# Optimization experiments

Measured on AMD Instinct MI355X. Metric: run time of the kernel, lower is better.

Reference implementation:

```python
import jax, jax.numpy as jnp
import numpy as np

D_MODEL = 768
N_HEAD = 12
N_BR = 4
DH = D_MODEL // N_HEAD          # 64
H_TOT = N_BR * N_HEAD           # 48
K_TOP = 4
B, T = 2, 1024


def setup_inputs() -> dict:
    key = jax.random.key(0)
    ks = jax.random.split(key, 16)
    s = 0.02
    return {
        "A": jax.random.normal(ks[0], (B, T, D_MODEL), jnp.float32),
        "X": jax.random.normal(ks[1], (B, T, D_MODEL), jnp.float32),
        "WK_w": jax.random.normal(ks[2], (D_MODEL, D_MODEL), jnp.float32) * s,
        "WK_b": jax.random.normal(ks[3], (D_MODEL,), jnp.float32) * s,
        "WQ_w": jax.random.normal(ks[4], (D_MODEL * N_BR, D_MODEL), jnp.float32) * s,
        "wedge_A": jax.random.normal(ks[5], (DH, DH), jnp.float32) * s,
        "wedge_bias": jax.random.normal(ks[6], (H_TOT, DH), jnp.float32) * s,
        "sink": jax.random.normal(ks[7], (H_TOT,), jnp.float32) * s,
        "v_nulls": jax.random.normal(ks[8], (N_BR, D_MODEL), jnp.float32) * s,
        "V1_w": jax.random.normal(ks[9], (4 * DH, DH), jnp.float32) * s,
        "V1_b": jax.random.normal(ks[10], (4 * DH,), jnp.float32) * s,
        "V2_w": jax.random.normal(ks[11], (DH, 4 * DH), jnp.float32) * s,
        "V2_b": jax.random.normal(ks[12], (DH,), jnp.float32) * s,
        "WO_w": jax.random.normal(ks[13], (N_BR, D_MODEL, D_MODEL), jnp.float32) * s,
        "WO_b": jax.random.normal(ks[14], (N_BR, D_MODEL), jnp.float32) * s,
    }


def _wedge(x, wedge_A, wedge_bias):
    # S = (A - A^T) + diag_embed(id_bias); x: [B,H,T,Dh]
    skew = wedge_A - wedge_A.T                       # [Dh,Dh]
    S = skew[None, :, :] + jax.vmap(jnp.diag)(wedge_bias)  # [H,Dh,Dh]
    return x + jnp.einsum('bhtd,hde->bhte', x, S)


def _rope(x):
    # x: [B,H,T,Dh]; halves are interleaved-split then concatenated
    t_len = x.shape[2]
    inv_freq = 1.0 / (10000.0 ** (jnp.arange(0, DH, 2, dtype=jnp.float32) / DH))
    freqs = jnp.arange(t_len, dtype=jnp.float32)[:, None] * inv_freq[None, :]  # [T,Dh/2]
    cos = jnp.cos(freqs)[None, None]
    sin = jnp.sin(freqs)[None, None]
    x1 = x[..., 0::2]
    x2 = x[..., 1::2]
    return jnp.concatenate((-x2 * sin + x1 * cos, x1 * sin + x2 * cos), axis=-1)


def reference(A, X, WK_w, WK_b, WQ_w, wedge_A, wedge_bias, sink, v_nulls,
              V1_w, V1_b, V2_w, V2_b, WO_w, WO_b):
    b, t, c = A.shape
    scale = DH ** -0.5

    q = (A @ WQ_w.T).reshape(b, t, H_TOT, DH).transpose(0, 2, 1, 3)     # [B,Htot,T,Dh]
    k_base = X @ WK_w.T + WK_b
    k = k_base.reshape(b, t, N_HEAD, DH).transpose(0, 2, 1, 3)          # [B,Nsh,T,Dh]
    k = jnp.tile(k, (1, N_BR, 1, 1))                                    # [B,Htot,T,Dh]

    q = _rope(_wedge(q, wedge_A, wedge_bias))
    k = _rope(_wedge(k, wedge_A, wedge_bias))

    scores = jnp.einsum('bhtd,bhsd->bhts', q, k) * scale                # [B,Htot,T,T]
    causal = jnp.triu(jnp.ones((t, t), dtype=bool), k=1)
    scores = jnp.where(causal[None, None], -jnp.inf, scores)

    sinks = jnp.broadcast_to(sink.reshape(1, H_TOT, 1, 1), (b, H_TOT, t, 1))
    probs_full = jax.nn.softmax(jnp.concatenate([scores, sinks], axis=-1), axis=-1)
    probs_tokens = probs_full[..., :t]
    probs_sink = probs_full[..., t:]                                    # [B,Htot,T,1]

    k_top = min(K_TOP, t)
    vals, idxs = jax.lax.top_k(probs_tokens, k_top)                     # [B,Htot,T,K]
    weights = vals / (jnp.sum(vals, axis=-1, keepdims=True) + 1e-9)

    # gather top-k keys: [B,Htot,T,K,Dh]
    k_selected = jnp.take_along_axis(k[:, :, None, :, :], idxs[..., None], axis=3)
    marker = jnp.einsum('bhtk,bhtkd->bhtd', weights, k_selected)        # [B,Htot,T,Dh]

    h = jax.nn.gelu(marker @ V1_w.T + V1_b, approximate=False)
    out_tokens = h @ V2_w.T + V2_b                                      # [B,Htot,T,Dh]

    v_null = v_nulls.reshape(H_TOT, DH)[None, :, None, :]
    context = out_tokens + probs_sink * v_null                          # [B,Htot,T,Dh]

    context = context.reshape(b, N_BR, N_HEAD, t, DH)
    context = context.transpose(0, 1, 3, 2, 4).reshape(b, N_BR, t, c)   # [B,Nbr,T,C]

    y = jnp.einsum('bntc,ncd->bntd', context, WO_w) + WO_b[None, :, None, :]
    return y.mean(axis=1)
```

## Files before the change

### kernel.cpp

```cpp
#include <hip/hip_runtime.h>
#include <math.h>

constexpr int Bq  = 2;
constexpr int Tq  = 1024;
constexpr int HTq = 48;
constexpr float SCALE = 0.125f;
constexpr float EOFF = 8.0f;

typedef __attribute__((ext_vector_type(8))) short short8;
typedef __attribute__((ext_vector_type(4))) float f32x4;

__device__ inline unsigned short f2bf(float x) {
    unsigned u = __float_as_uint(x);
    return (unsigned short)((u + 0x7FFF + ((u >> 16) & 1)) >> 16);
}

__device__ inline unsigned umax_(unsigned a, unsigned b) { return a > b ? a : b; }
__device__ inline unsigned umin_(unsigned a, unsigned b) { return a > b ? b : a; }

__device__ inline void gload_lds16(const unsigned short* g, unsigned short* l) {
    __builtin_amdgcn_global_load_lds(
        (const __attribute__((address_space(1))) void*)g,
        (__attribute__((address_space(3))) void*)l,
        16, 0, 0);
}

__device__ inline void split3(float x, unsigned short& p0, unsigned short& p1, unsigned short& p2) {
    p0 = f2bf(x);
    float f0 = __uint_as_float((unsigned)p0 << 16);
    float r0 = x - f0;
    p1 = f2bf(r0);
    float f1 = __uint_as_float((unsigned)p1 << 16);
    float r1 = r0 - f1;
    p2 = f2bf(r1);
}

__device__ inline float gelu_f(float x) {
    float z = 0.70710678118654752f * x;
    float az = fabsf(z);
    float t = __frcp_rn(1.0f + 0.3275911f * az);
    float poly = t * (0.254829592f + t * (-0.284496736f + t * (1.421413741f
               + t * (-1.453152027f + t * 1.061405429f))));
    float er = 1.0f - poly * __expf(-az * az);
    er = (z < 0.0f) ? -er : er;
    return 0.5f * x * (1.0f + er);
}

__global__ void trig_kbias_kernel(float* __restrict__ trig,
                                  const float* __restrict__ WKb,
                                  const float* __restrict__ wA,
                                  float* __restrict__ bcat,
                                  const float* __restrict__ V1w,
                                  const float* __restrict__ V2w,
                                  unsigned short* __restrict__ vb16) {
    int i = blockIdx.x * 256 + threadIdx.x;
    int t = i >> 5, f = i & 31;
    float invf = powf(10000.0f, -(float)f * (1.0f / 32.0f));
    float ang = (float)t * invf;
    trig[i] = cosf(ang);
    trig[32768 + i] = sinf(ang);
    if (i < 768) {
        int hb = i >> 6, el = i & 63;
        float acc = 0.0f;
        for (int d = 0; d < 64; d++) {
            float sk = wA[d * 64 + el] - wA[el * 64 + d];
            acc += WKb[hb * 64 + d] * sk;
        }
        bcat[i] = WKb[i] + acc;
    } else if (i < 1536) {
        bcat[i] = WKb[i - 768];
    }
    if (i < 8192) {
        float4 v = (i < 4096) ? ((const float4*)V1w)[i] : ((const float4*)V2w)[i - 4096];
        ushort4 o;
        o.x = f2bf(v.x); o.y = f2bf(v.y); o.z = f2bf(v.z); o.w = f2bf(v.w);
        ((ushort4*)vb16)[i] = o;
    }
}

__global__ __launch_bounds__(256) void fold_split_kernel(
    const float* __restrict__ WQw, const float* __restrict__ WKw,
    const float* __restrict__ wA, const float* __restrict__ wbias,
    unsigned short* __restrict__ Wsp)
{
    const size_t WPL = (size_t)4608 * 768;
    __shared__ float sw[64][132];
    __shared__ float sk[64][65];
    int hb_ = blockIdx.x;
    int mode = (hb_ < 48) ? 0 : 1;
    int h = mode ? hb_ - 48 : hb_;
    const float* Wsrc = mode ? WKw : WQw;
    int cb = blockIdx.y;
    int tid = threadIdx.x;
    const float* Wh = Wsrc + (size_t)h * 64 * 768 + cb * 128;
    for (int l = tid; l < 64 * 32; l += 256) {
        int d = l >> 5, c4 = l & 31;
        *(float4*)&sw[d][c4 * 4] = *(const float4*)(Wh + (size_t)d * 768 + c4 * 4);
    }
    for (int l = tid; l < 4096; l += 256) {
        int d = l >> 6, e = l & 63;
        sk[d][e] = wA[l] - wA[e * 64 + d];
    }
    __syncthreads();
    int tx = tid & 15, ty = tid >> 4;
    float acc4[4][8] = {};
    for (int d = 0; d < 64; d++) {
        float s0 = sk[d][ty * 4 + 0], s1 = sk[d][ty * 4 + 1];
        float s2 = sk[d][ty * 4 + 2], s3 = sk[d][ty * 4 + 3];
        float w_[8];
        *(float4*)&w_[0] = *(const float4*)&sw[d][tx * 8];
        *(float4*)&w_[4] = *(const float4*)&sw[d][tx * 8 + 4];
        #pragma unroll
        for (int j = 0; j < 8; j++) {
            acc4[0][j] += s0 * w_[j];
            acc4[1][j] += s1 * w_[j];
            acc4[2][j] += s2 * w_[j];
            acc4[3][j] += s3 * w_[j];
        }
    }
    #pragma unroll
    for (int i = 0; i < 4; i++) {
        int e = ty * 4 + i;
        float scale = (mode == 0) ? (1.0f + wbias[h * 64 + e]) : 1.0f;
        size_t row = (mode == 0) ? (size_t)(h * 64 + e) : (size_t)(3072 + h * 64 + e);
        #pragma unroll
        for (int j = 0; j < 8; j++) {
            int cl = tx * 8 + j;
            float wv = sw[e][cl] * scale + acc4[i][j];
            unsigned short p0, p1, p2;
            split3(wv, p0, p1, p2);
            size_t idx = row * 768 + cb * 128 + cl;
            Wsp[idx] = p0; Wsp[WPL + idx] = p1; Wsp[2 * WPL + idx] = p2;
        }
        if (mode == 1) {
            size_t row2 = (size_t)(3840 + h * 64 + e);
            #pragma unroll
            for (int j = 0; j < 8; j++) {
                int cl = tx * 8 + j;
                unsigned short p0, p1, p2;
                split3(sw[e][cl], p0, p1, p2);
                size_t idx = row2 * 768 + cb * 128 + cl;
                Wsp[idx] = p0; Wsp[WPL + idx] = p1; Wsp[2 * WPL + idx] = p2;
            }
        }
    }
}

__global__ void split_act_kernel(const float* __restrict__ A, const float* __restrict__ X,
                                 unsigned short* __restrict__ Asp, unsigned short* __restrict__ Xsp)
{
    const size_t APL = (size_t)2048 * 768;
    int i = blockIdx.x * 256 + threadIdx.x;
    if (i >= 393216) return;
    float4 va = ((const float4*)A)[i];
    float4 vx = ((const float4*)X)[i];
    ushort4 a0, a1, a2, x0, x1, x2;
    split3(va.x, a0.x, a1.x, a2.x); split3(va.y, a0.y, a1.y, a2.y);
    split3(va.z, a0.z, a1.z, a2.z); split3(va.w, a0.w, a1.w, a2.w);
    split3(vx.x, x0.x, x1.x, x2.x); split3(vx.y, x0.y, x1.y, x2.y);
    split3(vx.z, x0.z, x1.z, x2.z); split3(vx.w, x0.w, x1.w, x2.w);
    ((ushort4*)(Asp))[i] = a0;
    ((ushort4*)(Asp + APL))[i] = a1;
    ((ushort4*)(Asp + 2 * APL))[i] = a2;
    ((ushort4*)(Xsp))[i] = x0;
    ((ushort4*)(Xsp + APL))[i] = x1;
    ((ushort4*)(Xsp + 2 * APL))[i] = x2;
}

__global__ __launch_bounds__(512) void proj_mfma_kernel(
    const unsigned short* __restrict__ Asp, const unsigned short* __restrict__ Xsp,
    const unsigned short* __restrict__ Wsp, const float* __restrict__ bcat,
    const float* __restrict__ trig, float* __restrict__ Qr, float* __restrict__ O2)
{
    const size_t APL = (size_t)2048 * 768;
    const size_t WPL = (size_t)4608 * 768;
    __shared__ unsigned short sA[3 * 128 * 32];
    __shared__ unsigned short sB[3 * 128 * 32];
    int bid = blockIdx.x;
    int swz = (bid & 7) * 72 + (bid >> 3);
    int nb = swz >> 4;
    int mb = swz & 15;
    bool isQ = (nb < 24);
    const unsigned short* Ab = isQ ? Asp : Xsp;
    int m0 = mb * 128, n0 = nb * 128;
    int tid = threadIdx.x;
    int w = tid >> 6, lane = tid & 63;
    int wm = w & 1, wn = w >> 1;
    int rf = lane & 15, kg = lane >> 4;
    int mbase = m0 + wm * 64;

    int srcslot = (lane & 3) ^ ((lane >> 3) & 3);
    const unsigned short* gsrcA[3];
    const unsigned short* gsrcB[3];
    unsigned short* ldstA[3];
    unsigned short* ldstB[3];
    #pragma unroll
    for (int i = 0; i < 3; i++) {
        int reg = w + i * 8;
        int p = reg >> 3, rg = reg & 7;
        int row = rg * 16 + (lane >> 2);
        gsrcA[i] = Ab  + (size_t)p * APL + (size_t)(m0 + row) * 768 + srcslot * 8;
        gsrcB[i] = Wsp + (size_t)p * WPL + (size_t)(n0 + row) * 768 + srcslot * 8;
        ldstA[i] = &sA[p * 4096 + rg * 512];
        ldstB[i] = &sB[p * 4096 + rg * 512];
    }

    f32x4 acc[4][2] = {};
    for (int k0 = 0; k0 < 768; k0 += 32) {
        __syncthreads();
        #pragma unroll
        for (int i = 0; i < 3; i++) {
            gload_lds16(gsrcA[i] + k0, ldstA[i]);
            gload_lds16(gsrcB[i] + k0, ldstB[i]);
        }
        __syncthreads();

        short8 a0[4], a1[4], a2[4], b0[2], b1[2], b2[2];
        #pragma unroll
        for (int mi = 0; mi < 4; mi++) {
            int row = wm * 64 + mi * 16 + rf;
            a0[mi] = *(const short8*)&sA[0 * 4096 + row * 32 + ((kg ^ ((row >> 1) & 3)) * 8)];
        }
        #pragma unroll
        for (int nj = 0; nj < 2; nj++) {
            int row = wn * 32 + nj * 16 + rf;
            b0[nj] = *(const short8*)&sB[0 * 4096 + row * 32 + ((kg ^ ((row >> 1) & 3)) * 8)];
        }
        #pragma unroll
        for (int mi = 0; mi < 4; mi++)
            #pragma unroll
            for (int nj = 0; nj < 2; nj++)
                acc[mi][nj] = __builtin_amdgcn_mfma_f32_16x16x32_bf16(a0[mi], b0[nj], acc[mi][nj], 0, 0, 0);
        #pragma unroll
        for (int nj = 0; nj < 2; nj++) {
            int row = wn * 32 + nj * 16 + rf;
            b1[nj] = *(const short8*)&sB[1 * 4096 + row * 32 + ((kg ^ ((row >> 1) & 3)) * 8)];
        }
        #pragma unroll
        for (int mi = 0; mi < 4; mi++)
            #pragma unroll
            for (int nj = 0; nj < 2; nj++)
                acc[mi][nj] = __builtin_amdgcn_mfma_f32_16x16x32_bf16(a0[mi], b1[nj], acc[mi][nj], 0, 0, 0);
        #pragma unroll
        for (int nj = 0; nj < 2; nj++) {
            int row = wn * 32 + nj * 16 + rf;
            b2[nj] = *(const short8*)&sB[2 * 4096 + row * 32 + ((kg ^ ((row >> 1) & 3)) * 8)];
        }
        #pragma unroll
        for (int mi = 0; mi < 4; mi++)
            #pragma unroll
            for (int nj = 0; nj < 2; nj++)
                acc[mi][nj] = __builtin_amdgcn_mfma_f32_16x16x32_bf16(a0[mi], b2[nj], acc[mi][nj], 0, 0, 0);
        #pragma unroll
        for (int mi = 0; mi < 4; mi++) {
            int row = wm * 64 + mi * 16 + rf;
            a1[mi] = *(const short8*)&sA[1 * 4096 + row * 32 + ((kg ^ ((row >> 1) & 3)) * 8)];
        }
        #pragma unroll
        for (int mi = 0; mi < 4; mi++)
            #pragma unroll
            for (int nj = 0; nj < 2; nj++)
                acc[mi][nj] = __builtin_amdgcn_mfma_f32_16x16x32_bf16(a1[mi], b0[nj], acc[mi][nj], 0, 0, 0);
        #pragma unroll
        for (int mi = 0; mi < 4; mi++)
            #pragma unroll
            for (int nj = 0; nj < 2; nj++)
                acc[mi][nj] = __builtin_amdgcn_mfma_f32_16x16x32_bf16(a1[mi], b1[nj], acc[mi][nj], 0, 0, 0);
        #pragma unroll
        for (int mi = 0; mi < 4; mi++) {
            int row = wm * 64 + mi * 16 + rf;
            a2[mi] = *(const short8*)&sA[2 * 4096 + row * 32 + ((kg ^ ((row >> 1) & 3)) * 8)];
        }
        #pragma unroll
        for (int mi = 0; mi < 4; mi++)
            #pragma unroll
            for (int nj = 0; nj < 2; nj++)
                acc[mi][nj] = __builtin_amdgcn_mfma_f32_16x16x32_bf16(a2[mi], b0[nj], acc[mi][nj], 0, 0, 0);
    }

    if (isQ) {
        #pragma unroll
        for (int mi = 0; mi < 4; mi++) {
            #pragma unroll
            for (int r = 0; r < 4; r++) {
                int m = mbase + mi * 16 + kg * 4 + r;
                int b_ = m >> 10, t = m & 1023;
                #pragma unroll
                for (int nj = 0; nj < 2; nj++) {
                    int col_local = wn * 32 + nj * 16 + rf;
                    int h = nb * 2 + (col_local >> 6);
                    int d = col_local & 63;
                    int i = d >> 1;
                    float v = acc[mi][nj][r];
                    float pv = __shfl_xor(v, 1);
                    float c = trig[t * 32 + i];
                    float s = trig[32768 + t * 32 + i];
                    float outv = (rf & 1) ? (pv * s + v * c) : (v * c - pv * s);
                    int col = (rf & 1) ? (32 + i) : i;
                    size_t base = ((size_t)(b_ * 48 + h) * 1024 + t) * 64;
                    Qr[base + col] = outv;
                }
            }
        }
    } else {
        #pragma unroll
        for (int nj = 0; nj < 2; nj++) {
            int col = (n0 - 3072) + wn * 32 + nj * 16 + rf;
            float bv = bcat[col];
            #pragma unroll
            for (int mi = 0; mi < 4; mi++)
                #pragma unroll
                for (int r = 0; r < 4; r++) {
                    int m = mbase + mi * 16 + kg * 4 + r;
                    O2[(size_t)m * 1536 + col] = acc[mi][nj][r] + bv;
                }
        }
    }
}

__global__ void k_finish_kernel(const float* __restrict__ O2, const float* __restrict__ trig,
                                const float* __restrict__ wbias,
                                float* __restrict__ Kr, unsigned short* __restrict__ Kb16)
{
    int idx = blockIdx.x * 256 + threadIdx.x;
    int pr = idx & 31;
    int tmp = idx >> 5;
    int hb = tmp % 12;
    int bt = tmp / 12;
    int t = bt & 1023, b = bt >> 10;
    const float* yx = O2 + (size_t)bt * 1536 + hb * 64 + pr * 2;
    float y0 = yx[0], y1 = yx[1];
    float x0 = yx[768], x1 = yx[769];
    float cv = trig[t * 32 + pr], sv = trig[32768 + t * 32 + pr];
    #pragma unroll
    for (int r = 0; r < 4; r++) {
        int h = hb + 12 * r;
        float b0 = wbias[h * 64 + 2 * pr], b1 = wbias[h * 64 + 2 * pr + 1];
        float wz0 = y0 + x0 * b0;
        float wz1 = y1 + x1 * b1;
        float lo = wz0 * cv - wz1 * sv;
        float hi = wz0 * sv + wz1 * cv;
        size_t base = ((size_t)(b * 48 + h) * 1024 + t) * 64;
        Kr[base + pr] = lo;
        Kr[base + 32 + pr] = hi;
        Kb16[base + pr] = f2bf(lo);
        Kb16[base + 32 + pr] = f2bf(hi);
    }
}

__global__ __launch_bounds__(256, 4) void attn_mfma_topk_kernel(
    const float* __restrict__ Qr, const float* __restrict__ Kr,
    const unsigned short* __restrict__ Kb, const float* __restrict__ sink,
    unsigned short* __restrict__ markerb, float* __restrict__ psink)
{
    const int bh = blockIdx.x;
    const int y  = blockIdx.y;
    const int w = threadIdx.x >> 6, lane = threadIdx.x & 63;
    const int rf = lane & 15, kg = lane >> 4;
    const int h = bh % HTq;
    const size_t rowbase = (size_t)bh * Tq;
    const unsigned short* Kbb = Kb + rowbase * 64;
    const float sk = sink[h];

    #pragma unroll 1
    for (int g = 0; g < 2; g++) {
        const int qb = g ? y : 15 - y;
        const int q0 = qb * 64 + w * 16;

        short8 a0, a1;
        {
            const float* qp = Qr + (rowbase + q0 + rf) * 64 + kg * 8;
            float4 u0 = *(const float4*)qp;
            float4 u1 = *(const float4*)(qp + 4);
            float4 u2 = *(const float4*)(qp + 32);
            float4 u3 = *(const float4*)(qp + 36);
            a0[0]=(short)f2bf(u0.x); a0[1]=(short)f2bf(u0.y); a0[2]=(short)f2bf(u0.z); a0[3]=(short)f2bf(u0.w);
            a0[4]=(short)f2bf(u1.x); a0[5]=(short)f2bf(u1.y); a0[6]=(short)f2bf(u1.z); a0[7]=(short)f2bf(u1.w);
            a1[0]=(short)f2bf(u2.x); a1[1]=(short)f2bf(u2.y); a1[2]=(short)f2bf(u2.z); a1[3]=(short)f2bf(u2.w);
            a1[4]=(short)f2bf(u3.x); a1[5]=(short)f2bf(u3.y); a1[6]=(short)f2bf(u3.z); a1[7]=(short)f2bf(u3.w);
        }

        float Z_[4];
        unsigned t_[4][4];
        #pragma unroll
        for (int r = 0; r < 4; r++) {
            Z_[r] = 0.0f;
            t_[r][0] = 0u; t_[r][1] = 0u; t_[r][2] = 0u; t_[r][3] = 0u;
        }

        short8 cA0[4], cA1[4], cB0[4], cB1[4];
        {
            const unsigned short* p = Kbb + (size_t)rf * 64 + kg * 8;
            #pragma unroll
            for (int kc = 0; kc < 4; kc++) {
                cA0[kc] = *(const short8*)(p + kc * 1024);
                cA1[kc] = *(const short8*)(p + kc * 1024 + 32);
            }
        }

        auto body = [&](short8 (&cb0)[4], short8 (&cb1)[4],
                        short8 (&nb0)[4], short8 (&nb1)[4], int tile) {
            f32x4 accs[4];
            __builtin_amdgcn_s_setprio(1);
            #pragma unroll
            for (int kc = 0; kc < 4; kc++) {
                f32x4 acc = {0.f, 0.f, 0.f, 0.f};
                acc = __builtin_amdgcn_mfma_f32_16x16x32_bf16(a0, cb0[kc], acc, 0, 0, 0);
                acc = __builtin_amdgcn_mfma_f32_16x16x32_bf16(a1, cb1[kc], acc, 0, 0, 0);
                accs[kc] = acc;
            }
            __builtin_amdgcn_s_setprio(0);
            const unsigned short* np = Kbb + (size_t)((tile + 1) * 64 + rf) * 64 + kg * 8;
            #pragma unroll
            for (int kc = 0; kc < 4; kc++) {
                nb0[kc] = *(const short8*)(np + kc * 1024);
                nb1[kc] = *(const short8*)(np + kc * 1024 + 32);
            }
            const int s0 = tile << 6;
            #pragma unroll
            for (int r = 0; r < 4; r++) {
                float s8[4];
                #pragma unroll
                for (int kc = 0; kc < 4; kc++) s8[kc] = fmaf(accs[kc][r], SCALE, -EOFF);
                #pragma unroll
                for (int kc = 0; kc < 4; kc++) {
                    unsigned u = __float_as_uint(s8[kc]);
                    unsigned key = u ^ ((unsigned)(((int)u) >> 31) | 0x80000000u);
                    unsigned c = (key & 0xFFFFFC00u) | (unsigned)(s0 + kc * 16 + rf);
                    unsigned n;
                    n = umax_(t_[r][0], c);  c = umin_(t_[r][0], c);  t_[r][0] = n;
                    n = umax_(t_[r][1], c);  c = umin_(t_[r][1], c);  t_[r][1] = n;
                    n = umax_(t_[r][2], c);  c = umin_(t_[r][2], c);  t_[r][2] = n;
                    t_[r][3] = umax_(t_[r][3], c);
                }
                float e0 = __expf(s8[0]), e1 = __expf(s8[1]);
                float e2 = __expf(s8[2]), e3 = __expf(s8[3]);
                Z_[r] += (e0 + e1) + (e2 + e3);
            }
        };

        int tile = 0;
        for (; tile + 1 < qb; tile += 2) {
            body(cA0, cA1, cB0, cB1, tile);
            body(cB0, cB1, cA0, cA1, tile + 1);
        }
        if (tile < qb) {
            body(cA0, cA1, cB0, cB1, tile);
            #pragma unroll
            for (int kc = 0; kc < 4; kc++) { cA0[kc] = cB0[kc]; cA1[kc] = cB1[kc]; }
        }

        {
            f32x4 accs[4];
            __builtin_amdgcn_s_setprio(1);
            #pragma unroll
            for (int kc = 0; kc < 4; kc++) {
                f32x4 acc = {0.f, 0.f, 0.f, 0.f};
                acc = __builtin_amdgcn_mfma_f32_16x16x32_bf16(a0, cA0[kc], acc, 0, 0, 0);
                acc = __builtin_amdgcn_mfma_f32_16x16x32_bf16(a1, cA1[kc], acc, 0, 0, 0);
                accs[kc] = acc;
            }
            __builtin_amdgcn_s_setprio(0);
            const int s0 = qb << 6;
            #pragma unroll
            for (int r = 0; r < 4; r++) {
                const int trow = q0 + kg * 4 + r;
                float ev[4];
                #pragma unroll
                for (int kc = 0; kc < 4; kc++) {
                    int k = s0 + kc * 16 + rf;
                    bool ok = (k <= trow);
                    float s8 = fmaf(accs[kc][r], SCALE, -EOFF);
                    unsigned u = __float_as_uint(s8);
                    unsigned key = u ^ ((unsigned)(((int)u) >> 31) | 0x80000000u);
                    unsigned c = (key & 0xFFFFFC00u) | (unsigned)k;
                    c = ok ? c : 0u;
                    unsigned n;
                    n = umax_(t_[r][0], c);  c = umin_(t_[r][0], c);  t_[r][0] = n;
                    n = umax_(t_[r][1], c);  c = umin_(t_[r][1], c);  t_[r][1] = n;
                    n = umax_(t_[r][2], c);  c = umin_(t_[r][2], c);  t_[r][2] = n;
                    t_[r][3] = umax_(t_[r][3], c);
                    ev[kc] = ok ? __expf(s8) : 0.0f;
                }
                Z_[r] += (ev[0] + ev[1]) + (ev[2] + ev[3]);
            }
        }

        const float esk = __expf(sk - EOFF);
        #pragma unroll 1
        for (int r = 0; r < 4; r++) {
            const int q = q0 + kg * 4 + r;
            float Z = Z_[r];
            #pragma unroll
            for (int off = 1; off < 16; off <<= 1) Z += __shfl_xor(Z, off);
            float Zf = Z + esk;

            unsigned e0, e1, e2, e3, e4, e5, e6, e7;
            {
                unsigned A0 = t_[r][0], A1 = t_[r][1], A2 = t_[r][2], A3 = t_[r][3];
                unsigned B0 = (unsigned)__shfl_xor((int)A0, 1);
                unsigned B1 = (unsigned)__shfl_xor((int)A1, 1);
                unsigned B2 = (unsigned)__shfl_xor((int)A2, 1);
                unsigned B3 = (unsigned)__shfl_xor((int)A3, 1);
                unsigned y0 = umax_(A0, B3), y4 = umin_(A0, B3);
                unsigned y1 = umax_(A1, B2), y5 = umin_(A1, B2);
                unsigned y2 = umax_(A2, B1), y6 = umin_(A2, B1);
                unsigned y3 = umax_(A3, B0), y7 = umin_(A3, B0);
                unsigned z0 = umax_(y0, y2), z2 = umin_(y0, y2);
                unsigned z1 = umax_(y1, y3), z3 = umin_(y1, y3);
                unsigned z4 = umax_(y4, y6), z6 = umin_(y4, y6);
                unsigned z5 = umax_(y5, y7), z7 = umin_(y5, y7);
                e0 = umax_(z0, z1); e1 = umin_(z0, z1);
                e2 = umax_(z2, z3); e3 = umin_(z2, z3);
                e4 = umax_(z4, z5); e5 = umin_(z4, z5);
                e6 = umax_(z6, z7); e7 = umin_(z6, z7);
            }
            auto merge8 = [&](int off) {
                unsigned f0 = (unsigned)__shfl_xor((int)e0, off);
                unsigned f1 = (unsigned)__shfl_xor((int)e1, off);
                unsigned f2 = (unsigned)__shfl_xor((int)e2, off);
                unsigned f3 = (unsigned)__shfl_xor((int)e3, off);
                unsigned f4 = (unsigned)__shfl_xor((int)e4, off);
                unsigned f5 = (unsigned)__shfl_xor((int)e5, off);
                unsigned f6 = (unsigned)__shfl_xor((int)e6, off);
                unsigned f7 = (unsigned)__shfl_xor((int)e7, off);
                unsigned m0 = umax_(e0, f7), m1 = umax_(e1, f6);
                unsigned m2 = umax_(e2, f5), m3 = umax_(e3, f4);
                unsigned m4 = umax_(e4, f3), m5 = umax_(e5, f2);
                unsigned m6 = umax_(e6, f1), m7 = umax_(e7, f0);
                unsigned p0 = umax_(m0, m4), p4 = umin_(m0, m4);
                unsigned p1 = umax_(m1, m5), p5 = umin_(m1, m5);
                unsigned p2 = umax_(m2, m6), p6 = umin_(m2, m6);
                unsigned p3 = umax_(m3, m7), p7 = umin_(m3, m7);
                unsigned q0_ = umax_(p0, p2), q2_ = umin_(p0, p2);
                unsigned q1_ = umax_(p1, p3), q3_ = umin_(p1, p3);
                unsigned q4_ = umax_(p4, p6), q6_ = umin_(p4, p6);
                unsigned q5_ = umax_(p5, p7), q7_ = umin_(p5, p7);
                e0 = umax_(q0_, q1_); e1 = umin_(q0_, q1_);
                e2 = umax_(q2_, q3_); e3 = umin_(q2_, q3_);
                e4 = umax_(q4_, q5_); e5 = umin_(q4_, q5_);
                e6 = umax_(q6_, q7_); e7 = umin_(q6_, q7_);
            };
            merge8(2); merge8(4); merge8(8);
            unsigned ck[8] = {e0, e1, e2, e3, e4, e5, e6, e7};

            const float4 qv = *(const float4*)(Qr + (rowbase + q) * 64 + rf * 4);
            float sc[8]; int ci[8];
            #pragma unroll
            for (int c = 0; c < 8; c++) {
                bool valid = (ck[c] != 0u);
                int idx = (int)(ck[c] & 1023u);
                int lidx = valid ? idx : 0;
                const float4 kv = *(const float4*)(Kr + (rowbase + lidx) * 64 + rf * 4);
                float p = qv.x * kv.x + qv.y * kv.y + qv.z * kv.z + qv.w * kv.w;
                #pragma unroll
                for (int off = 1; off < 16; off <<= 1) p += __shfl_xor(p, off);
                sc[c] = valid ? p * SCALE : -1e30f;
                ci[c] = valid ? idx : -1;
            }
            float bv[4]; int bi[4];
            #pragma unroll
            for (int rd = 0; rd < 4; rd++) {
                float v = sc[0]; int id = ci[0];
                #pragma unroll
                for (int c = 1; c < 8; c++) {
                    bool take = (sc[c] > v) || ((sc[c] == v) && ((unsigned)ci[c] < (unsigned)id));
                    v = take ? sc[c] : v; id = take ? ci[c] : id;
                }
                bv[rd] = v; bi[rd] = id;
                #pragma unroll
                for (int c = 0; c < 8; c++) {
                    bool kill = (ci[c] == id) && (sc[c] == v);
                    sc[c] = kill ? -3e30f : sc[c];
                }
            }
            float e0f = __expf(bv[0] - EOFF), e1f = __expf(bv[1] - EOFF);
            float e2f = __expf(bv[2] - EOFF), e3f = __expf(bv[3] - EOFF);
            float wsum = e0f + e1f + e2f + e3f + Zf * 1e-9f;
            float w0 = e0f / wsum, w1 = e1f / wsum, w2 = e2f / wsum, w3 = e3f / wsum;
            int i0 = bi[0] < 0 ? 0 : bi[0];
            int i1 = bi[1] < 0 ? 0 : bi[1];
            int i2 = bi[2] < 0 ? 0 : bi[2];
            int i3 = bi[3] < 0 ? 0 : bi[3];
            const float4 k0 = *(const float4*)(Kr + (rowbase + i0) * 64 + rf * 4);
            const float4 k1 = *(const float4*)(Kr + (rowbase + i1) * 64 + rf * 4);
            const float4 k2 = *(const float4*)(Kr + (rowbase + i2) * 64 + rf * 4);
            const float4 k3 = *(const float4*)(Kr + (rowbase + i3) * 64 + rf * 4);
            float mx = w0 * k0.x + w1 * k1.x + w2 * k2.x + w3 * k3.x;
            float my = w0 * k0.y + w1 * k1.y + w2 * k2.y + w3 * k3.y;
            float mz = w0 * k0.z + w1 * k1.z + w2 * k2.z + w3 * k3.z;
            float mw = w0 * k0.w + w1 * k1.w + w2 * k2.w + w3 * k3.w;
            ushort4 mo;
            mo.x = f2bf(mx); mo.y = f2bf(my); mo.z = f2bf(mz); mo.w = f2bf(mw);
            *(ushort4*)(markerb + (rowbase + q) * 64 + rf * 4) = mo;
            if (rf == 0) psink[rowbase + q] = esk / Zf;
        }
    }
}

__global__ __launch_bounds__(256) void wo_transpose_kernel(
    const float* __restrict__ WOw, unsigned short* __restrict__ WOt)
{
    __shared__ float tl[64][65];
    int tid = threadIdx.x;
    int n = blockIdx.z;
    int c0 = blockIdx.x * 64, d0 = blockIdx.y * 64;
    const float* src = WOw + (size_t)n * 768 * 768;
    for (int l = tid; l < 64 * 16; l += 256) {
        int r = l >> 4, q = l & 15;
        float4 v = *(const float4*)(src + (size_t)(c0 + r) * 768 + d0 + q * 4);
        tl[r][q * 4 + 0] = v.x; tl[r][q * 4 + 1] = v.y;
        tl[r][q * 4 + 2] = v.z; tl[r][q * 4 + 3] = v.w;
    }
    __syncthreads();
    for (int l = tid; l < 64 * 16; l += 256) {
        int d = l >> 4, q = l & 15;
        ushort4 o;
        o.x = f2bf(tl[q * 4 + 0][d]); o.y = f2bf(tl[q * 4 + 1][d]);
        o.z = f2bf(tl[q * 4 + 2][d]); o.w = f2bf(tl[q * 4 + 3][d]);
        *(ushort4*)(WOt + (size_t)n * 768 * 768 + (size_t)(d0 + d) * 768 + c0 + q * 4) = o;
    }
}

__global__ __launch_bounds__(256) void mlp_mfma_kernel(
    const unsigned short* __restrict__ markerb, const float* __restrict__ psink,
    const unsigned short* __restrict__ V1b16, const float* __restrict__ V1bias,
    const unsigned short* __restrict__ V2b16, const float* __restrict__ V2bias,
    const float* __restrict__ vnulls, unsigned short* __restrict__ ctxb)
{
    __shared__ float h_lds[4][16][65];
    int tid = threadIdx.x;
    int w = tid >> 6, lane = tid & 63;
    int rf = lane & 15, kg = lane >> 4;
    size_t r0 = (size_t)blockIdx.x * 64 + 16 * w;

    short8 a1[2];
    #pragma unroll
    for (int kk = 0; kk < 2; kk++)
        a1[kk] = *(const short8*)(markerb + (r0 + rf) * 64 + kk * 32 + kg * 8);

    f32x4 acc2[4] = {};
    for (int ch = 0; ch < 4; ch++) {
        f32x4 acc1[4] = {};
        __builtin_amdgcn_s_setprio(1);
        #pragma unroll
        for (int nj = 0; nj < 4; nj++)
            #pragma unroll
            for (int kk = 0; kk < 2; kk++) {
                short8 b1 = *(const short8*)(V1b16 + (size_t)(ch * 64 + nj * 16 + rf) * 64 + kk * 32 + kg * 8);
                acc1[nj] = __builtin_amdgcn_mfma_f32_16x16x32_bf16(a1[kk], b1, acc1[nj], 0, 0, 0);
            }
        __builtin_amdgcn_s_setprio(0);
        #pragma unroll
        for (int nj = 0; nj < 4; nj++) {
            float bb = V1bias[ch * 64 + nj * 16 + rf];
            #pragma unroll
            for (int r = 0; r < 4; r++) {
                float x = acc1[nj][r] + bb;
                h_lds[w][kg * 4 + r][nj * 16 + rf] = gelu_f(x);
            }
        }
        #pragma unroll
        for (int kk = 0; kk < 2; kk++) {
            const float* hp = &h_lds[w][rf][kk * 32 + kg * 8];
            float4 p0 = *(const float4*)hp;
            float4 p1 = *(const float4*)(hp + 4);
            short8 a2;
            a2[0] = (short)f2bf(p0.x); a2[1] = (short)f2bf(p0.y);
            a2[2] = (short)f2bf(p0.z); a2[3] = (short)f2bf(p0.w);
            a2[4] = (short)f2bf(p1.x); a2[5] = (short)f2bf(p1.y);
            a2[6] = (short)f2bf(p1.z); a2[7] = (short)f2bf(p1.w);
            __builtin_amdgcn_s_setprio(1);
            #pragma unroll
            for (int njo = 0; njo < 4; njo++) {
                short8 b2 = *(const short8*)(V2b16 + (size_t)(njo * 16 + rf) * 256 + ch * 64 + kk * 32 + kg * 8);
                acc2[njo] = __builtin_amdgcn_mfma_f32_16x16x32_bf16(a2, b2, acc2[njo], 0, 0, 0);
            }
            __builtin_amdgcn_s_setprio(0);
        }
    }
    #pragma unroll
    for (int r = 0; r < 4; r++) {
        size_t R = r0 + kg * 4 + r;
        int bh = (int)(R >> 10), t = (int)(R & 1023);
        int b = bh / 48, h = bh % 48;
        int n = h / 12, head = h % 12;
        float ps = psink[R];
        size_t base = ((size_t)((b * 4 + n) * 1024 + t)) * 768 + head * 64;
        #pragma unroll
        for (int njo = 0; njo < 4; njo++) {
            int d = njo * 16 + rf;
            float v = acc2[njo][r] + V2bias[d] + ps * vnulls[h * 64 + d];
            ctxb[base + d] = f2bf(v);
        }
    }
}

__global__ __launch_bounds__(256) void gemm_wo_mfma(
    const unsigned short* __restrict__ ctxb, const unsigned short* __restrict__ WOtb,
    const float* __restrict__ WOb, float* __restrict__ Out)
{
    __shared__ unsigned short sA[64 * 128];
    __shared__ unsigned short sB[64 * 128];
    int tid = threadIdx.x;
    int w = tid >> 6, lane = tid & 63;
    int wm = w >> 1, wn = w & 1;
    int rf = lane & 15, kg = lane >> 4;
    int m0 = blockIdx.x * 64, n0 = blockIdx.y * 64;
    int b = m0 >> 10, t0 = m0 & 1023;
    f32x4 acc[2][2] = {};
    for (int n = 0; n < 4; n++) {
        const unsigned short* Ab = ctxb + ((size_t)((b * 4 + n) * 1024 + t0)) * 768;
        const unsigned short* Bb = WOtb + (size_t)n * 768 * 768 + (size_t)n0 * 768;
        for (int k0 = 0; k0 < 768; k0 += 128) {
            __syncthreads();
            #pragma unroll
            for (int j = 0; j < 4; j++) {
                int e = tid + j * 256;
                int r = e >> 4, s = e & 15;
                int ss = s ^ (r & 15);
                *(short8*)&sA[r * 128 + ss * 8] = *(const short8*)(Ab + (size_t)r * 768 + k0 + s * 8);
                *(short8*)&sB[r * 128 + ss * 8] = *(const short8*)(Bb + (size_t)r * 768 + k0 + s * 8);
            }
            __syncthreads();
            __builtin_amdgcn_s_setprio(1);
            #pragma unroll
            for (int kk = 0; kk < 4; kk++) {
                int slot = kk * 4 + kg;
                int rA0 = wm * 32 + rf, rA1 = wm * 32 + 16 + rf;
                int rB0 = wn * 32 + rf, rB1 = wn * 32 + 16 + rf;
                short8 a0v = *(const short8*)&sA[rA0 * 128 + ((slot ^ (rA0 & 15)) * 8)];
                short8 a1v = *(const short8*)&sA[rA1 * 128 + ((slot ^ (rA1 & 15)) * 8)];
                short8 b0v = *(const short8*)&sB[rB0 * 128 + ((slot ^ (rB0 & 15)) * 8)];
                short8 b1v = *(const short8*)&sB[rB1 * 128 + ((slot ^ (rB1 & 15)) * 8)];
                acc[0][0] = __builtin_amdgcn_mfma_f32_16x16x32_bf16(a0v, b0v, acc[0][0], 0, 0, 0);
                acc[0][1] = __builtin_amdgcn_mfma_f32_16x16x32_bf16(a0v, b1v, acc[0][1], 0, 0, 0);
                acc[1][0] = __builtin_amdgcn_mfma_f32_16x16x32_bf16(a1v, b0v, acc[1][0], 0, 0, 0);
                acc[1][1] = __builtin_amdgcn_mfma_f32_16x16x32_bf16(a1v, b1v, acc[1][1], 0, 0, 0);
            }
            __builtin_amdgcn_s_setprio(0);
        }
    }
    #pragma unroll
    for (int nj = 0; nj < 2; nj++) {
        int col = n0 + wn * 32 + nj * 16 + rf;
        float bm = WOb[col] + WOb[768 + col] + WOb[1536 + col] + WOb[2304 + col];
        #pragma unroll
        for (int mi = 0; mi < 2; mi++)
            #pragma unroll
            for (int r = 0; r < 4; r++) {
                int row = m0 + wm * 32 + mi * 16 + kg * 4 + r;
                Out[(size_t)row * 768 + col] = 0.25f * (acc[mi][nj][r] + bm);
            }
    }
}

extern "C" void kernel_launch(void* const* d_in, const int* in_sizes, int n_in,
                              void* d_out, int out_size, void* d_ws, size_t ws_size,
                              hipStream_t stream) {
    const float* A      = (const float*)d_in[0];
    const float* X      = (const float*)d_in[1];
    const float* WKw    = (const float*)d_in[2];
    const float* WKb    = (const float*)d_in[3];
    const float* WQw    = (const float*)d_in[4];
    const float* wA     = (const float*)d_in[5];
    const float* wB     = (const float*)d_in[6];
    const float* sink   = (const float*)d_in[7];
    const float* vnulls = (const float*)d_in[8];
    const float* V1w    = (const float*)d_in[9];
    const float* V1b    = (const float*)d_in[10];
    const float* V2w    = (const float*)d_in[11];
    const float* V2b    = (const float*)d_in[12];
    const float* WOw    = (const float*)d_in[13];
    const float* WOb    = (const float*)d_in[14];
    float* out = (float*)d_out;
    (void)in_sizes; (void)n_in; (void)out_size; (void)ws_size;

    float* ws = (float*)d_ws;
    size_t off = 0;
    float* Qr   = ws + off;  off += 6291456;
    float* Kr   = ws + off;  off += 6291456;
    float* trig = ws + off;  off += 65536;
    float* bcat = ws + off;  off += 2048;
    float* O2   = ws + off;  off += 3145728;
    float* Wsp_f = ws + off; off += 5308416;
    unsigned short* Wsp = (unsigned short*)Wsp_f;
    unsigned short* Asp = (unsigned short*)(ws + off); off += 2359296;
    unsigned short* Xsp = (unsigned short*)(ws + off); off += 2359296;
    unsigned short* V1b16 = (unsigned short*)(ws + off); off += 16384;
    unsigned short* V2b16 = V1b16 + 16384;
    unsigned short* markerb = (unsigned short*)O2;
    unsigned short* Kb16 = Wsp;
    float* psink = Wsp_f + 3145728;
    unsigned short* WOtb  = Asp;
    unsigned short* ctxb  = (unsigned short*)Qr;

    trig_kbias_kernel<<<128, 256, 0, stream>>>(trig, WKb, wA, bcat, V1w, V2w, V1b16);
    fold_split_kernel<<<dim3(60, 6), 256, 0, stream>>>(WQw, WKw, wA, wB, Wsp);
    split_act_kernel<<<1536, 256, 0, stream>>>(A, X, Asp, Xsp);
    proj_mfma_kernel<<<576, 512, 0, stream>>>(Asp, Xsp, Wsp, bcat, trig, Qr, O2);
    k_finish_kernel<<<3072, 256, 0, stream>>>(O2, trig, wB, Kr, Kb16);
    attn_mfma_topk_kernel<<<dim3(96, 8), 256, 0, stream>>>(Qr, Kr, Kb16, sink, markerb, psink);
    wo_transpose_kernel<<<dim3(12, 12, 4), 256, 0, stream>>>(WOw, WOtb);
    mlp_mfma_kernel<<<1536, 256, 0, stream>>>(markerb, psink, V1b16, V1b, V2b16, V2b, vnulls, ctxb);
    gemm_wo_mfma<<<dim3(32, 12), 256, 0, stream>>>(ctxb, WOtb, WOb, out);
}
```

Measured before the change: 315.8 us.

## Merge prep kernels into one launch and double-buffer projection GEMM LDS

Three small preprocessing kernels (trig/bias, weight fold-split, activation split) are merged into a single launch that dispatches work by block index, removing two launches and the gaps between them. The projection MFMA GEMM gains double-buffered LDS, so the async global-to-LDS load of the next K tile is issued before computing the current one, cutting one barrier per iteration. MFMA runs are bracketed with s_setprio to favor issue. LDS use doubles, which may reduce occupancy of the 512-thread blocks.

```diff
diff --git a/kernel.cpp b/kernel.cpp
--- a/kernel.cpp
+++ b/kernel.cpp
@@ -46,125 +46,126 @@
     return 0.5f * x * (1.0f + er);
 }
 
-__global__ void trig_kbias_kernel(float* __restrict__ trig,
-                                  const float* __restrict__ WKb,
-                                  const float* __restrict__ wA,
-                                  float* __restrict__ bcat,
-                                  const float* __restrict__ V1w,
-                                  const float* __restrict__ V2w,
-                                  unsigned short* __restrict__ vb16) {
-    int i = blockIdx.x * 256 + threadIdx.x;
-    int t = i >> 5, f = i & 31;
-    float invf = powf(10000.0f, -(float)f * (1.0f / 32.0f));
-    float ang = (float)t * invf;
-    trig[i] = cosf(ang);
-    trig[32768 + i] = sinf(ang);
-    if (i < 768) {
-        int hb = i >> 6, el = i & 63;
-        float acc = 0.0f;
-        for (int d = 0; d < 64; d++) {
-            float sk = wA[d * 64 + el] - wA[el * 64 + d];
-            acc += WKb[hb * 64 + d] * sk;
-        }
-        bcat[i] = WKb[i] + acc;
-    } else if (i < 1536) {
-        bcat[i] = WKb[i - 768];
-    }
-    if (i < 8192) {
-        float4 v = (i < 4096) ? ((const float4*)V1w)[i] : ((const float4*)V2w)[i - 4096];
-        ushort4 o;
-        o.x = f2bf(v.x); o.y = f2bf(v.y); o.z = f2bf(v.z); o.w = f2bf(v.w);
-        ((ushort4*)vb16)[i] = o;
-    }
-}
-
-__global__ __launch_bounds__(256) void fold_split_kernel(
+__global__ __launch_bounds__(256) void prep_kernel(
+    float* __restrict__ trig, const float* __restrict__ WKb,
+    const float* __restrict__ wA, float* __restrict__ bcat,
+    const float* __restrict__ V1w, const float* __restrict__ V2w,
+    unsigned short* __restrict__ vb16,
     const float* __restrict__ WQw, const float* __restrict__ WKw,
-    const float* __restrict__ wA, const float* __restrict__ wbias,
-    unsigned short* __restrict__ Wsp)
+    const float* __restrict__ wbias, unsigned short* __restrict__ Wsp,
+    const float* __restrict__ A, const float* __restrict__ X,
+    unsigned short* __restrict__ Asp, unsigned short* __restrict__ Xsp)
 {
     const size_t WPL = (size_t)4608 * 768;
+    const size_t APL = (size_t)2048 * 768;
     __shared__ float sw[64][132];
     __shared__ float sk[64][65];
-    int hb_ = blockIdx.x;
-    int mode = (hb_ < 48) ? 0 : 1;
-    int h = mode ? hb_ - 48 : hb_;
-    const float* Wsrc = mode ? WKw : WQw;
-    int cb = blockIdx.y;
+    int bid = blockIdx.x;
     int tid = threadIdx.x;
-    const float* Wh = Wsrc + (size_t)h * 64 * 768 + cb * 128;
-    for (int l = tid; l < 64 * 32; l += 256) {
-        int d = l >> 5, c4 = l & 31;
-        *(float4*)&sw[d][c4 * 4] = *(const float4*)(Wh + (size_t)d * 768 + c4 * 4);
-    }
-    for (int l = tid; l < 4096; l += 256) {
-        int d = l >> 6, e = l & 63;
-        sk[d][e] = wA[l] - wA[e * 64 + d];
-    }
-    __syncthreads();
-    int tx = tid & 15, ty = tid >> 4;
-    float acc4[4][8] = {};
-    for (int d = 0; d < 64; d++) {
-        float s0 = sk[d][ty * 4 + 0], s1 = sk[d][ty * 4 + 1];
-        float s2 = sk[d][ty * 4 + 2], s3 = sk[d][ty * 4 + 3];
-        float w_[8];
-        *(float4*)&w_[0] = *(const float4*)&sw[d][tx * 8];
-        *(float4*)&w_[4] = *(const float4*)&sw[d][tx * 8 + 4];
-        #pragma unroll
-        for (int j = 0; j < 8; j++) {
-            acc4[0][j] += s0 * w_[j];
-            acc4[1][j] += s1 * w_[j];
-            acc4[2][j] += s2 * w_[j];
-            acc4[3][j] += s3 * w_[j];
-        }
-    }
-    #pragma unroll
-    for (int i = 0; i < 4; i++) {
-        int e = ty * 4 + i;
-        float scale = (mode == 0) ? (1.0f + wbias[h * 64 + e]) : 1.0f;
-        size_t row = (mode == 0) ? (size_t)(h * 64 + e) : (size_t)(3072 + h * 64 + e);
-        #pragma unroll
-        for (int j = 0; j < 8; j++) {
-            int cl = tx * 8 + j;
-            float wv = sw[e][cl] * scale + acc4[i][j];
-            unsigned short p0, p1, p2;
-            split3(wv, p0, p1, p2);
-            size_t idx = row * 768 + cb * 128 + cl;
-            Wsp[idx] = p0; Wsp[WPL + idx] = p1; Wsp[2 * WPL + idx] = p2;
-        }
-        if (mode == 1) {
-            size_t row2 = (size_t)(3840 + h * 64 + e);
+
+    if (bid < 128) {
+        int i = bid * 256 + tid;
+        int t = i >> 5, f = i & 31;
+        float invf = powf(10000.0f, -(float)f * (1.0f / 32.0f));
+        float ang = (float)t * invf;
+        trig[i] = cosf(ang);
+        trig[32768 + i] = sinf(ang);
+        if (i < 768) {
+            int hb = i >> 6, el = i & 63;
+            float acc = 0.0f;
+            for (int d = 0; d < 64; d++) {
+                float s = wA[d * 64 + el] - wA[el * 64 + d];
+                acc += WKb[hb * 64 + d] * s;
+            }
+            bcat[i] = WKb[i] + acc;
+        } else if (i < 1536) {
+            bcat[i] = WKb[i - 768];
+        }
+        if (i < 8192) {
+            float4 v = (i < 4096) ? ((const float4*)V1w)[i] : ((const float4*)V2w)[i - 4096];
+            ushort4 o;
+            o.x = f2bf(v.x); o.y = f2bf(v.y); o.z = f2bf(v.z); o.w = f2bf(v.w);
+            ((ushort4*)vb16)[i] = o;
+        }
+        return;
+    }
+    if (bid < 488) {
+        int id = bid - 128;
+        int hb_ = id / 6, cb = id % 6;
+        int mode = (hb_ < 48) ? 0 : 1;
+        int h = mode ? hb_ - 48 : hb_;
+        const float* Wsrc = mode ? WKw : WQw;
+        const float* Wh = Wsrc + (size_t)h * 64 * 768 + cb * 128;
+        for (int l = tid; l < 64 * 32; l += 256) {
+            int d = l >> 5, c4 = l & 31;
+            *(float4*)&sw[d][c4 * 4] = *(const float4*)(Wh + (size_t)d * 768 + c4 * 4);
+        }
+        for (int l = tid; l < 4096; l += 256) {
+            int d = l >> 6, e = l & 63;
+            sk[d][e] = wA[l] - wA[e * 64 + d];
+        }
+        __syncthreads();
+        int tx = tid & 15, ty = tid >> 4;
+        float acc4[4][8] = {};
+        for (int d = 0; d < 64; d++) {
+            float s0 = sk[d][ty * 4 + 0], s1 = sk[d][ty * 4 + 1];
+            float s2 = sk[d][ty * 4 + 2], s3 = sk[d][ty * 4 + 3];
+            float w_[8];
+            *(float4*)&w_[0] = *(const float4*)&sw[d][tx * 8];
+            *(float4*)&w_[4] = *(const float4*)&sw[d][tx * 8 + 4];
+            #pragma unroll
+            for (int j = 0; j < 8; j++) {
+                acc4[0][j] += s0 * w_[j];
+                acc4[1][j] += s1 * w_[j];
+                acc4[2][j] += s2 * w_[j];
+                acc4[3][j] += s3 * w_[j];
+            }
+        }
+        #pragma unroll
+        for (int i = 0; i < 4; i++) {
+            int e = ty * 4 + i;
+            float scale = (mode == 0) ? (1.0f + wbias[h * 64 + e]) : 1.0f;
+            size_t row = (mode == 0) ? (size_t)(h * 64 + e) : (size_t)(3072 + h * 64 + e);
             #pragma unroll
             for (int j = 0; j < 8; j++) {
                 int cl = tx * 8 + j;
+                float wv = sw[e][cl] * scale + acc4[i][j];
                 unsigned short p0, p1, p2;
-                split3(sw[e][cl], p0, p1, p2);
-                size_t idx = row2 * 768 + cb * 128 + cl;
+                split3(wv, p0, p1, p2);
+                size_t idx = row * 768 + cb * 128 + cl;
                 Wsp[idx] = p0; Wsp[WPL + idx] = p1; Wsp[2 * WPL + idx] = p2;
             }
-        }
-    }
-}
-
-__global__ void split_act_kernel(const float* __restrict__ A, const float* __restrict__ X,
-                                 unsigned short* __restrict__ Asp, unsigned short* __restrict__ Xsp)
-{
-    const size_t APL = (size_t)2048 * 768;
-    int i = blockIdx.x * 256 + threadIdx.x;
-    if (i >= 393216) return;
-    float4 va = ((const float4*)A)[i];
-    float4 vx = ((const float4*)X)[i];
-    ushort4 a0, a1, a2, x0, x1, x2;
-    split3(va.x, a0.x, a1.x, a2.x); split3(va.y, a0.y, a1.y, a2.y);
-    split3(va.z, a0.z, a1.z, a2.z); split3(va.w, a0.w, a1.w, a2.w);
-    split3(vx.x, x0.x, x1.x, x2.x); split3(vx.y, x0.y, x1.y, x2.y);
-    split3(vx.z, x0.z, x1.z, x2.z); split3(vx.w, x0.w, x1.w, x2.w);
-    ((ushort4*)(Asp))[i] = a0;
-    ((ushort4*)(Asp + APL))[i] = a1;
-    ((ushort4*)(Asp + 2 * APL))[i] = a2;
-    ((ushort4*)(Xsp))[i] = x0;
-    ((ushort4*)(Xsp + APL))[i] = x1;
-    ((ushort4*)(Xsp + 2 * APL))[i] = x2;
+            if (mode == 1) {
+                size_t row2 = (size_t)(3840 + h * 64 + e);
+                #pragma unroll
+                for (int j = 0; j < 8; j++) {
+                    int cl = tx * 8 + j;
+                    unsigned short p0, p1, p2;
+                    split3(sw[e][cl], p0, p1, p2);
+                    size_t idx = row2 * 768 + cb * 128 + cl;
+                    Wsp[idx] = p0; Wsp[WPL + idx] = p1; Wsp[2 * WPL + idx] = p2;
+                }
+            }
+        }
+        return;
+    }
+    {
+        int i = (bid - 488) * 256 + tid;
+        if (i >= 393216) return;
+        float4 va = ((const float4*)A)[i];
+        float4 vx = ((const float4*)X)[i];
+        ushort4 a0, a1, a2, x0, x1, x2;
+        split3(va.x, a0.x, a1.x, a2.x); split3(va.y, a0.y, a1.y, a2.y);
+        split3(va.z, a0.z, a1.z, a2.z); split3(va.w, a0.w, a1.w, a2.w);
+        split3(vx.x, x0.x, x1.x, x2.x); split3(vx.y, x0.y, x1.y, x2.y);
+        split3(vx.z, x0.z, x1.z, x2.z); split3(vx.w, x0.w, x1.w, x2.w);
+        ((ushort4*)(Asp))[i] = a0;
+        ((ushort4*)(Asp + APL))[i] = a1;
+        ((ushort4*)(Asp + 2 * APL))[i] = a2;
+        ((ushort4*)(Xsp))[i] = x0;
+        ((ushort4*)(Xsp + APL))[i] = x1;
+        ((ushort4*)(Xsp + 2 * APL))[i] = x2;
+    }
 }
 
 __global__ __launch_bounds__(512) void proj_mfma_kernel(
@@ -174,8 +175,9 @@
 {
     const size_t APL = (size_t)2048 * 768;
     const size_t WPL = (size_t)4608 * 768;
-    __shared__ unsigned short sA[3 * 128 * 32];
-    __shared__ unsigned short sB[3 * 128 * 32];
+    const int BUFO = 3 * 128 * 32;
+    __shared__ unsigned short sA[2 * 3 * 128 * 32];
+    __shared__ unsigned short sB[2 * 3 * 128 * 32];
     int bid = blockIdx.x;
     int swz = (bid & 7) * 72 + (bid >> 3);
     int nb = swz >> 4;
@@ -205,57 +207,71 @@
         ldstB[i] = &sB[p * 4096 + rg * 512];
     }
 
+    auto stage = [&](int bs, int k0) {
+        #pragma unroll
+        for (int i = 0; i < 3; i++) {
+            gload_lds16(gsrcA[i] + k0, ldstA[i] + bs * BUFO);
+            gload_lds16(gsrcB[i] + k0, ldstB[i] + bs * BUFO);
+        }
+    };
+
     f32x4 acc[4][2] = {};
-    for (int k0 = 0; k0 < 768; k0 += 32) {
-        __syncthreads();
-        #pragma unroll
-        for (int i = 0; i < 3; i++) {
-            gload_lds16(gsrcA[i] + k0, ldstA[i]);
-            gload_lds16(gsrcB[i] + k0, ldstB[i]);
-        }
-        __syncthreads();
-
+    stage(0, 0);
+    __syncthreads();
+    int cur = 0;
+    for (int step = 0; step < 24; step++) {
+        if (step < 23) stage(cur ^ 1, (step + 1) * 32);
+
+        const unsigned short* bA = &sA[cur * BUFO];
+        const unsigned short* bB = &sB[cur * BUFO];
         short8 a0[4], a1[4], a2[4], b0[2], b1[2], b2[2];
         #pragma unroll
         for (int mi = 0; mi < 4; mi++) {
             int row = wm * 64 + mi * 16 + rf;
-            a0[mi] = *(const short8*)&sA[0 * 4096 + row * 32 + ((kg ^ ((row >> 1) & 3)) * 8)];
+            a0[mi] = *(const short8*)&bA[0 * 4096 + row * 32 + ((kg ^ ((row >> 1) & 3)) * 8)];
         }
         #pragma unroll
         for (int nj = 0; nj < 2; nj++) {
             int row = wn * 32 + nj * 16 + rf;
-            b0[nj] = *(const short8*)&sB[0 * 4096 + row * 32 + ((kg ^ ((row >> 1) & 3)) * 8)];
-        }
+            b0[nj] = *(const short8*)&bB[0 * 4096 + row * 32 + ((kg ^ ((row >> 1) & 3)) * 8)];
+        }
+        __builtin_amdgcn_s_setprio(1);
         #pragma unroll
         for (int mi = 0; mi < 4; mi++)
             #pragma unroll
             for (int nj = 0; nj < 2; nj++)
                 acc[mi][nj] = __builtin_amdgcn_mfma_f32_16x16x32_bf16(a0[mi], b0[nj], acc[mi][nj], 0, 0, 0);
+        __builtin_amdgcn_s_setprio(0);
         #pragma unroll
         for (int nj = 0; nj < 2; nj++) {
             int row = wn * 32 + nj * 16 + rf;
-            b1[nj] = *(const short8*)&sB[1 * 4096 + row * 32 + ((kg ^ ((row >> 1) & 3)) * 8)];
-        }
+            b1[nj] = *(const short8*)&bB[1 * 4096 + row * 32 + ((kg ^ ((row >> 1) & 3)) * 8)];
+        }
+        __builtin_amdgcn_s_setprio(1);
         #pragma unroll
         for (int mi = 0; mi < 4; mi++)
             #pragma unroll
             for (int nj = 0; nj < 2; nj++)
                 acc[mi][nj] = __builtin_amdgcn_mfma_f32_16x16x32_bf16(a0[mi], b1[nj], acc[mi][nj], 0, 0, 0);
+        __builtin_amdgcn_s_setprio(0);
         #pragma unroll
         for (int nj = 0; nj < 2; nj++) {
             int row = wn * 32 + nj * 16 + rf;
-            b2[nj] = *(const short8*)&sB[2 * 4096 + row * 32 + ((kg ^ ((row >> 1) & 3)) * 8)];
-        }
+            b2[nj] = *(const short8*)&bB[2 * 4096 + row * 32 + ((kg ^ ((row >> 1) & 3)) * 8)];
+        }
+        __builtin_amdgcn_s_setprio(1);
         #pragma unroll
         for (int mi = 0; mi < 4; mi++)
             #pragma unroll
             for (int nj = 0; nj < 2; nj++)
                 acc[mi][nj] = __builtin_amdgcn_mfma_f32_16x16x32_bf16(a0[mi], b2[nj], acc[mi][nj], 0, 0, 0);
+        __builtin_amdgcn_s_setprio(0);
         #pragma unroll
         for (int mi = 0; mi < 4; mi++) {
             int row = wm * 64 + mi * 16 + rf;
-            a1[mi] = *(const short8*)&sA[1 * 4096 + row * 32 + ((kg ^ ((row >> 1) & 3)) * 8)];
-        }
+            a1[mi] = *(const short8*)&bA[1 * 4096 + row * 32 + ((kg ^ ((row >> 1) & 3)) * 8)];
+        }
+        __builtin_amdgcn_s_setprio(1);
         #pragma unroll
         for (int mi = 0; mi < 4; mi++)
             #pragma unroll
@@ -266,16 +282,22 @@
             #pragma unroll
             for (int nj = 0; nj < 2; nj++)
                 acc[mi][nj] = __builtin_amdgcn_mfma_f32_16x16x32_bf16(a1[mi], b1[nj], acc[mi][nj], 0, 0, 0);
+        __builtin_amdgcn_s_setprio(0);
         #pragma unroll
         for (int mi = 0; mi < 4; mi++) {
             int row = wm * 64 + mi * 16 + rf;
-            a2[mi] = *(const short8*)&sA[2 * 4096 + row * 32 + ((kg ^ ((row >> 1) & 3)) * 8)];
-        }
+            a2[mi] = *(const short8*)&bA[2 * 4096 + row * 32 + ((kg ^ ((row >> 1) & 3)) * 8)];
+        }
+        __builtin_amdgcn_s_setprio(1);
         #pragma unroll
         for (int mi = 0; mi < 4; mi++)
             #pragma unroll
             for (int nj = 0; nj < 2; nj++)
                 acc[mi][nj] = __builtin_amdgcn_mfma_f32_16x16x32_bf16(a2[mi], b0[nj], acc[mi][nj], 0, 0, 0);
+        __builtin_amdgcn_s_setprio(0);
+
+        __syncthreads();
+        cur ^= 1;
     }
 
     if (isQ) {
@@ -795,9 +817,8 @@
     unsigned short* WOtb  = Asp;
     unsigned short* ctxb  = (unsigned short*)Qr;
 
-    trig_kbias_kernel<<<128, 256, 0, stream>>>(trig, WKb, wA, bcat, V1w, V2w, V1b16);
-    fold_split_kernel<<<dim3(60, 6), 256, 0, stream>>>(WQw, WKw, wA, wB, Wsp);
-    split_act_kernel<<<1536, 256, 0, stream>>>(A, X, Asp, Xsp);
+    prep_kernel<<<2024, 256, 0, stream>>>(trig, WKb, wA, bcat, V1w, V2w, V1b16,
+                                          WQw, WKw, wB, Wsp, A, X, Asp, Xsp);
     proj_mfma_kernel<<<576, 512, 0, stream>>>(Asp, Xsp, Wsp, bcat, trig, Qr, O2);
     k_finish_kernel<<<3072, 256, 0, stream>>>(O2, trig, wB, Kr, Kb16);
     attn_mfma_topk_kernel<<<dim3(96, 8), 256, 0, stream>>>(Qr, Kr, Kb16, sink, markerb, psink);
```

After: 328.8 us. +4.1%, slower.
